# Optimization experiments

Measured on AMD Instinct MI355X. Metric: run time of the kernel, lower is better.

## Reference

```python
import jax, jax.numpy as jnp
import numpy as np

B, S, D, H = 2, 2048, 1024, 16
HD = D // H               # head_dim = input_size / num_heads
STEPS = 1                 # update_steps_max extra Hopfield update steps
LN_EPS = 1e-5
SCALING = 1.0 / np.sqrt(HD)  # beta = 1/sqrt(head_dim)


def layernorm(x, g, b):
    m = x.mean(-1, keepdims=True)
    v = ((x - m) ** 2).mean(-1, keepdims=True)
    return (x - m) * jax.lax.rsqrt(v + LN_EPS) * g + b


def setup_inputs() -> dict:
    key = jax.random.key(0)
    ks = jax.random.split(key, 9)
    s = 0.02
    f32 = jnp.float32
    return {
        "data": jax.random.normal(ks[0], (B, S, D), f32),
        # affine LayerNorm params (stored / state / projection patterns)
        "g_k": jnp.ones((D,), f32), "b_k": jnp.zeros((D,), f32),
        "g_q": jnp.ones((D,), f32), "b_q": jnp.zeros((D,), f32),
        "g_v": jnp.ones((D,), f32), "b_v": jnp.zeros((D,), f32),
        # in-projections (q/k/v) and out-projection of HopfieldCore
        "Wq": jax.random.normal(ks[1], (D, D), f32) * s, "bq": jnp.zeros((D,), f32),
        "Wk": jax.random.normal(ks[2], (D, D), f32) * s, "bk": jnp.zeros((D,), f32),
        "Wv": jax.random.normal(ks[3], (D, D), f32) * s, "bv": jnp.zeros((D,), f32),
        "Wo": jax.random.normal(ks[4], (D, D), f32) * s, "bo": jnp.zeros((D,), f32),
    }


def reference(data, g_k, b_k, g_q, b_q, g_v, b_v,
              Wq, bq, Wk, bk, Wv, bv, Wo, bo):
    # single input tensor used as stored / state / projection pattern
    xk = layernorm(data, g_k, b_k)   # stored pattern  -> keys
    xq = layernorm(data, g_q, b_q)   # state pattern   -> queries
    xv = layernorm(data, g_v, b_v)   # pattern proj    -> values

    split = lambda t: t.reshape(B, S, H, HD).transpose(0, 2, 1, 3)  # [B,H,S,HD]
    q = split(xq @ Wq + bq)
    k = split(xk @ Wk + bk)
    v = split(xv @ Wv + bv)

    def assoc(q):  # xi = softmax(beta * q K^T)
        return jax.nn.softmax(
            jnp.einsum('bhqd,bhkd->bhqk', q, k) * SCALING, axis=-1)

    xi = assoc(q)
    for _ in range(STEPS):           # iterative Hopfield update: q <- xi K
        q = jnp.einsum('bhqk,bhkd->bhqd', xi, k)
        xi = assoc(q)

    out = jnp.einsum('bhqk,bhkd->bhqd', xi, v)        # retrieve with values
    out = out.transpose(0, 2, 1, 3).reshape(B, S, D)  # merge heads
    return out @ Wo + bo
```

## Files before the change

### kernel.cpp

```cpp
#include <hip/hip_runtime.h>
#include <hip/hip_bf16.h>

#define B_  2
#define S_  2048
#define D_  1024
#define H_  16
#define HD_ 64
#define M_  4096


typedef __attribute__((ext_vector_type(8))) short short8;
typedef __attribute__((ext_vector_type(4))) float f32x4;

#define CE_ 0.1803368801111204f
#define SD_ 56

typedef __attribute__((address_space(1))) const unsigned GU;
typedef __attribute__((address_space(3))) unsigned LU;
static __device__ __forceinline__ void glds16(const void* g, void* l){
  __builtin_amdgcn_global_load_lds((GU*)g, (LU*)l, 16, 0, 0);
}

static __device__ __forceinline__ unsigned short f2bfc(float f){
  union{float f; unsigned u;} c; c.f = f;
  return (unsigned short)((c.u + 0x8000u) >> 16);
}
static __device__ __forceinline__ unsigned pk2bf(float a, float b){
  union{float f; unsigned u;} ca, cb; ca.f=a; cb.f=b;
  return __builtin_amdgcn_perm(cb.u + 0x8000u, ca.u + 0x8000u, 0x07060302u);
}
static __device__ __forceinline__ unsigned pk2bft(float a, float b){
  union{float f; unsigned u;} ca, cb; ca.f=a; cb.f=b;
  return __builtin_amdgcn_perm(cb.u, ca.u, 0x07060302u);
}

__global__ __launch_bounds__(256) void prep_kernel(
  const float* __restrict__ data,
  const float* __restrict__ Wq, const float* __restrict__ Wk,
  const float* __restrict__ Wv, const float* __restrict__ Wo,
  const float* __restrict__ gq, const float* __restrict__ gk, const float* __restrict__ gv,
  const float* __restrict__ blq, const float* __restrict__ blk, const float* __restrict__ blv,
  const float* __restrict__ bpq, const float* __restrict__ bpk, const float* __restrict__ bpv,
  unsigned short* __restrict__ WT, unsigned short* __restrict__ xhat,
  float* __restrict__ bf)
{
  __shared__ unsigned short tile[64][72];
  __shared__ float red[4][64];
  int bid = blockIdx.x, t = threadIdx.x;
  if (bid < 1024){
    int z = bid >> 8, rem = bid & 255;
    int k0 = (rem>>4)*64, n0 = (rem&15)*64;
    const float* W = (z==0)?Wq:(z==1)?Wk:(z==2)?Wv:Wo;
    const float* g = (z==0)?gq:(z==1)?gk:(z==2)?gv:(const float*)0;
    unsigned short* out = WT + ((size_t)z<<20);
    {
      int kr = t>>2, c16 = (t&3)*16;
      float gs = g ? g[k0+kr]*((z==0)?CE_:1.0f) : 1.0f;
      const float* src = W + (size_t)(k0+kr)*D_ + n0 + c16;
      float4 w0 = *(const float4*)(src);
      float4 w1 = *(const float4*)(src+4);
      float4 w2 = *(const float4*)(src+8);
      float4 w3 = *(const float4*)(src+12);
      unsigned* tp = (unsigned*)&tile[kr][c16];
      tp[0]=pk2bf(w0.x*gs,w0.y*gs); tp[1]=pk2bf(w0.z*gs,w0.w*gs);
      tp[2]=pk2bf(w1.x*gs,w1.y*gs); tp[3]=pk2bf(w1.z*gs,w1.w*gs);
      tp[4]=pk2bf(w2.x*gs,w2.y*gs); tp[5]=pk2bf(w2.z*gs,w2.w*gs);
      tp[6]=pk2bf(w3.x*gs,w3.y*gs); tp[7]=pk2bf(w3.z*gs,w3.w*gs);
    }
    __syncthreads();
    {
      int nr = t>>2, kc = (t&3)*16;
      union { uint4 v[2]; unsigned short u[16]; } st;
      #pragma unroll
      for (int i=0;i<16;i++) st.u[i] = tile[kc+i][nr];
      unsigned short* dst = out + (size_t)(n0+nr)*D_ + k0 + kc;
      *(uint4*)(dst)     = st.v[0];
      *(uint4*)(dst + 8) = st.v[1];
    }
  } else if (bid < 2048){
    int row = (bid-1024)*4 + (t>>6);
    int l = t & 63;
    const float4* xr = (const float4*)(data + (size_t)row*D_);
    float4 v[4];
    float s = 0.f, ss = 0.f;
    #pragma unroll
    for (int i=0;i<4;i++){
      v[i] = xr[l + 64*i];
      s  += v[i].x+v[i].y+v[i].z+v[i].w;
      ss += v[i].x*v[i].x+v[i].y*v[i].y+v[i].z*v[i].z+v[i].w*v[i].w;
    }
    #pragma unroll
    for (int m=1;m<64;m<<=1){ s += __shfl_xor(s, m, 64); ss += __shfl_xor(ss, m, 64); }
    float me = s*(1.0f/D_);
    float var = ss*(1.0f/D_) - me*me;
    float rs = rsqrtf(var + 1e-5f);
    float nm = -me*rs;
    unsigned short* xo = xhat + (size_t)row*D_;
    #pragma unroll
    for (int i=0;i<4;i++){
      uint2 pk;
      pk.x = pk2bf(fmaf(v[i].x,rs,nm), fmaf(v[i].y,rs,nm));
      pk.y = pk2bf(fmaf(v[i].z,rs,nm), fmaf(v[i].w,rs,nm));
      *(uint2*)(xo + 4*l + 256*i) = pk;
    }
  } else {
    int idx = bid - 2048;
    int z = idx >> 4, xb = idx & 15;
    const float* W  = (z==0)?Wq:(z==1)?Wk:Wv;
    const float* bl = (z==0)?blq:(z==1)?blk:blv;
    const float* bp = (z==0)?bpq:(z==1)?bpk:bpv;
    int nl = t & 63, kg = t >> 6;
    int n = xb*64 + nl;
    float acc = 0.f;
    for (int k = kg*256; k < (kg+1)*256; k++)
      acc += bl[k] * W[(size_t)k*D_ + n];
    red[kg][nl] = acc;
    __syncthreads();
    if (t < 64){
      int nn = xb*64 + t;
      float v = red[0][t]+red[1][t]+red[2][t]+red[3][t] + bp[nn];
      bf[z*D_ + nn] = (z==0) ? v*CE_ : v;
    }
  }
}

__global__ __launch_bounds__(256) void gemm_qkv(
  const unsigned short* __restrict__ xhat,
  const unsigned short* __restrict__ WT,
  const float* __restrict__ biasf,
  unsigned short* __restrict__ qv, unsigned short* __restrict__ kb,
  unsigned short* __restrict__ kT, unsigned short* __restrict__ vT)
{
  int z = blockIdx.z;
  const unsigned short* Bt = WT + ((size_t)z<<20);
  const float* bias = biasf + z*D_;
  unsigned short* oN = (z==0)?qv:(z==1)?kb:(unsigned short*)0;
  unsigned short* oT = (z==0)?(unsigned short*)0:(z==1)?kT:vT;

  __shared__ __align__(16) unsigned short As[128*32];
  __shared__ __align__(16) unsigned short Bs[128*32];
  int tid = threadIdx.x, w = tid>>6, l = tid&63;
  int m0 = blockIdx.x*128, n0 = blockIdx.y*128;
  int wr = (w>>1)*64, wc = (w&1)*64;
  int lr = l&15, qd = l>>4;

  const unsigned short* gA = xhat + (size_t)(m0 + w*32 + (l>>2))*D_ + (l&3)*8;
  const unsigned short* gB = Bt   + (size_t)(n0 + w*32 + (l>>2))*D_ + (l&3)*8;
  unsigned short* lA0 = &As[(w*32)*32];
  unsigned short* lA1 = &As[(w*32+16)*32];
  unsigned short* lB0 = &Bs[(w*32)*32];
  unsigned short* lB1 = &Bs[(w*32+16)*32];

  const f32x4 fz = {0.f,0.f,0.f,0.f};
  f32x4 acc[4][4];
  #pragma unroll
  for (int i=0;i<4;i++)
    #pragma unroll
    for (int j=0;j<4;j++) acc[i][j] = fz;

  for (int kk=0; kk<D_; kk+=32){
    __syncthreads();
    glds16(gA + kk,                 lA0);
    glds16(gA + kk + (size_t)16*D_, lA1);
    glds16(gB + kk,                 lB0);
    glds16(gB + kk + (size_t)16*D_, lB1);
    __syncthreads();
    short8 af[4], bfr[4];
    #pragma unroll
    for (int i=0;i<4;i++) af[i]  = *(const short8*)(As + (wr + i*16 + lr)*32 + qd*8);
    #pragma unroll
    for (int j=0;j<4;j++) bfr[j] = *(const short8*)(Bs + (wc + j*16 + lr)*32 + qd*8);
    #pragma unroll
    for (int i=0;i<4;i++)
      #pragma unroll
      for (int j=0;j<4;j++)
        acc[i][j] = __builtin_amdgcn_mfma_f32_16x16x32_bf16(af[i], bfr[j], acc[i][j], 0, 0, 0);
  }

  #pragma unroll
  for (int j=0;j<4;j++){
    int n = n0 + wc + j*16 + lr;
    float bias_n = bias[n];
    #pragma unroll
    for (int i=0;i<4;i++){
      int mb = m0 + wr + i*16 + qd*4;
      float v0 = acc[i][j][0] + bias_n;
      float v1 = acc[i][j][1] + bias_n;
      float v2 = acc[i][j][2] + bias_n;
      float v3 = acc[i][j][3] + bias_n;
      if (oN){
        oN[(size_t)(mb+0)*D_ + n] = f2bfc(v0);
        oN[(size_t)(mb+1)*D_ + n] = f2bfc(v1);
        oN[(size_t)(mb+2)*D_ + n] = f2bfc(v2);
        oN[(size_t)(mb+3)*D_ + n] = f2bfc(v3);
      }
      if (oT){
        int bb = mb >> 11, sI = mb & (S_-1);
        int hh = n >> 6,  dd = n & 63;
        uint2 pk; pk.x = pk2bf(v0, v1); pk.y = pk2bf(v2, v3);
        *(uint2*)(oT + (size_t)((bb*H_ + hh)*HD_ + dd)*S_ + sI) = pk;
      }
    }
  }
}

__global__ __launch_bounds__(256) void gemm_out(
  const unsigned short* __restrict__ A,
  const unsigned short* __restrict__ Bt,
  const float* __restrict__ bo,
  float* __restrict__ Cf)
{
  __shared__ __align__(16) unsigned short As[128*32];
  __shared__ __align__(16) unsigned short Bs[128*32];
  int tid = threadIdx.x, w = tid>>6, l = tid&63;
  int m0 = blockIdx.x*128, n0 = blockIdx.y*128;
  int wr = (w>>1)*64, wc = (w&1)*64;
  int lr = l&15, qd = l>>4;

  const unsigned short* gA = A  + (size_t)(m0 + w*32 + (l>>2))*D_ + (l&3)*8;
  const unsigned short* gB = Bt + (size_t)(n0 + w*32 + (l>>2))*D_ + (l&3)*8;
  unsigned short* lA0 = &As[(w*32)*32];
  unsigned short* lA1 = &As[(w*32+16)*32];
  unsigned short* lB0 = &Bs[(w*32)*32];
  unsigned short* lB1 = &Bs[(w*32+16)*32];

  const f32x4 fz = {0.f,0.f,0.f,0.f};
  f32x4 acc[4][4];
  #pragma unroll
  for (int i=0;i<4;i++)
    #pragma unroll
    for (int j=0;j<4;j++) acc[i][j] = fz;

  for (int kk=0; kk<D_; kk+=32){
    __syncthreads();
    glds16(gA + kk,                 lA0);
    glds16(gA + kk + (size_t)16*D_, lA1);
    glds16(gB + kk,                 lB0);
    glds16(gB + kk + (size_t)16*D_, lB1);
    __syncthreads();
    short8 af[4], bfr[4];
    #pragma unroll
    for (int i=0;i<4;i++) af[i]  = *(const short8*)(As + (wr + i*16 + lr)*32 + qd*8);
    #pragma unroll
    for (int j=0;j<4;j++) bfr[j] = *(const short8*)(Bs + (wc + j*16 + lr)*32 + qd*8);
    #pragma unroll
    for (int i=0;i<4;i++)
      #pragma unroll
      for (int j=0;j<4;j++)
        acc[i][j] = __builtin_amdgcn_mfma_f32_16x16x32_bf16(af[i], bfr[j], acc[i][j], 0, 0, 0);
  }

  #pragma unroll
  for (int j=0;j<4;j++){
    int n = n0 + wc + j*16 + lr;
    float bias_n = bo[n];
    #pragma unroll
    for (int i=0;i<4;i++){
      int mb = m0 + wr + i*16 + qd*4;
      Cf[(size_t)(mb+0)*D_ + n] = acc[i][j][0] + bias_n;
      Cf[(size_t)(mb+1)*D_ + n] = acc[i][j][1] + bias_n;
      Cf[(size_t)(mb+2)*D_ + n] = acc[i][j][2] + bias_n;
      Cf[(size_t)(mb+3)*D_ + n] = acc[i][j][3] + bias_n;
    }
  }
}

__global__ __launch_bounds__(256) void attn_fused(
  unsigned short* __restrict__ QO,
  const unsigned short* __restrict__ K,
  const unsigned short* __restrict__ KT,
  const unsigned short* __restrict__ VT)
{
  int qt = blockIdx.x;
  int h  = blockIdx.y;
  int b  = qt >> 4;
  int bh = b*H_ + h;
  int tid = threadIdx.x, w = tid>>6, l = tid&63;
  int lr = l&15, qd = l>>4;
  int r8 = tid>>3, c8 = (tid&7)*8;
  int chf = c8>>5, co = c8&31;

  __shared__ __align__(16) unsigned short sK[2][64*SD_];
  __shared__ __align__(16) unsigned short sV[2][64*SD_];
  __shared__ __align__(16) unsigned short sP[4][2][16*SD_];

  const f32x4 fz = {0.f,0.f,0.f,0.f};

  unsigned short* Qbase = QO + (size_t)(qt*128 + w*32) * D_ + h*64;
  short8 qf[2][2];
  #pragma unroll
  for (int gg=0; gg<2; gg++)
    #pragma unroll
    for (int hf=0; hf<2; hf++)
      qf[gg][hf] = *(const short8*)(Qbase + (size_t)(gg*16+lr)*D_ + hf*32 + qd*8);

  const unsigned short* Khead = K + (size_t)(b*S_)*D_ + h*64;
  const unsigned short* Vh0 = KT + (size_t)bh*HD_*S_;
  const unsigned short* Vh1 = VT + (size_t)bh*HD_*S_;
  unsigned short* Pw0 = &sP[w][0][0];
  unsigned short* Pw1 = &sP[w][1][0];

  f32x4 oacc[2][4];
  float lac[2];

  uint4 kr0, kr1, vr0, vr1;
  {
    kr0 = *(const uint4*)(Khead + (size_t)(r8   )*D_ + c8);
    kr1 = *(const uint4*)(Khead + (size_t)(r8+32)*D_ + c8);
    vr0 = *(const uint4*)(Vh0 + (size_t)(r8   )*S_ + c8);
    vr1 = *(const uint4*)(Vh0 + (size_t)(r8+32)*S_ + c8);
  }

  #pragma unroll 1
  for (int phase=0; phase<2; phase++){
    const unsigned short* Vhead = phase ? Vh1 : Vh0;
    lac[0]=0.f; lac[1]=0.f;
    #pragma unroll
    for (int gg=0;gg<2;gg++)
      #pragma unroll
      for (int t=0;t<4;t++) oacc[gg][t]=fz;

    for (int kt=0; kt<S_; kt+=64){
      __syncthreads();
      *(uint4*)(&sK[chf][(r8   )*SD_ + co]) = kr0;
      *(uint4*)(&sK[chf][(r8+32)*SD_ + co]) = kr1;
      *(uint4*)(&sV[chf][(r8   )*SD_ + co]) = vr0;
      *(uint4*)(&sV[chf][(r8+32)*SD_ + co]) = vr1;
      __syncthreads();

      {
        int nkt = kt + 64;
        const unsigned short* Vn = Vhead;
        if (nkt >= S_){ nkt = 0; Vn = Vh1; }
        kr0 = *(const uint4*)(Khead + (size_t)(nkt+r8   )*D_ + c8);
        kr1 = *(const uint4*)(Khead + (size_t)(nkt+r8+32)*D_ + c8);
        vr0 = *(const uint4*)(Vn + (size_t)(r8   )*S_ + nkt + c8);
        vr1 = *(const uint4*)(Vn + (size_t)(r8+32)*S_ + nkt + c8);
      }

      f32x4 sc[2][4];
      #pragma unroll
      for (int st=0; st<4; st++){
        short8 kA0 = *(const short8*)(&sK[0][(st*16+lr)*SD_ + qd*8]);
        short8 kA1 = *(const short8*)(&sK[1][(st*16+lr)*SD_ + qd*8]);
        #pragma unroll
        for (int gg=0; gg<2; gg++){
          f32x4 z = fz;
          z = __builtin_amdgcn_mfma_f32_16x16x32_bf16(kA0, qf[gg][0], z, 0,0,0);
          z = __builtin_amdgcn_mfma_f32_16x16x32_bf16(kA1, qf[gg][1], z, 0,0,0);
          sc[gg][st] = z;
        }
      }
      short8 pf[2][2];
      #pragma unroll
      for (int gg=0; gg<2; gg++){
        #pragma unroll
        for (int st=0; st<4; st++){
          float p0=__builtin_amdgcn_exp2f(sc[gg][st][0]);
          float p1=__builtin_amdgcn_exp2f(sc[gg][st][1]);
          float p2=__builtin_amdgcn_exp2f(sc[gg][st][2]);
          float p3=__builtin_amdgcn_exp2f(sc[gg][st][3]);
          lac[gg] += (p0+p1)+(p2+p3);
          uint2 pk; pk.x = pk2bft(p0,p1); pk.y = pk2bft(p2,p3);
          unsigned short* Ph = (st&2) ? Pw1 : Pw0;
          *(uint2*)(Ph + lr*SD_ + (st&1)*16 + qd*4) = pk;
        }
        pf[gg][0] = *(const short8*)(Pw0 + lr*SD_ + qd*8);
        pf[gg][1] = *(const short8*)(Pw1 + lr*SD_ + qd*8);
      }
      #pragma unroll
      for (int dt=0; dt<4; dt++){
        short8 vA0 = *(const short8*)(&sV[0][(dt*16+lr)*SD_ + qd*8]);
        short8 vA1 = *(const short8*)(&sV[1][(dt*16+lr)*SD_ + qd*8]);
        #pragma unroll
        for (int gg=0; gg<2; gg++){
          oacc[gg][dt] = __builtin_amdgcn_mfma_f32_16x16x32_bf16(vA0, pf[gg][0], oacc[gg][dt], 0,0,0);
          oacc[gg][dt] = __builtin_amdgcn_mfma_f32_16x16x32_bf16(vA1, pf[gg][1], oacc[gg][dt], 0,0,0);
        }
      }
    }

    #pragma unroll
    for (int gg=0;gg<2;gg++){
      lac[gg] += __shfl_xor(lac[gg], 16, 64);
      lac[gg] += __shfl_xor(lac[gg], 32, 64);
    }

    if (phase==0){
      #pragma unroll
      for (int gg=0;gg<2;gg++){
        float iv = CE_ * __builtin_amdgcn_rcpf(lac[gg]);
        #pragma unroll
        for (int dt=0;dt<4;dt++){
          uint2 pk;
          pk.x = pk2bf(oacc[gg][dt][0]*iv, oacc[gg][dt][1]*iv);
          pk.y = pk2bf(oacc[gg][dt][2]*iv, oacc[gg][dt][3]*iv);
          unsigned short* Ph = (dt&2) ? Pw1 : Pw0;
          *(uint2*)(Ph + lr*SD_ + (dt&1)*16 + qd*4) = pk;
        }
        qf[gg][0] = *(const short8*)(Pw0 + lr*SD_ + qd*8);
        qf[gg][1] = *(const short8*)(Pw1 + lr*SD_ + qd*8);
      }
    } else {
      #pragma unroll
      for (int gg=0;gg<2;gg++){
        float iv = __builtin_amdgcn_rcpf(lac[gg]);
        unsigned short* Ob = QO + (size_t)(qt*128 + w*32 + gg*16 + lr)*D_ + h*64;
        #pragma unroll
        for (int dt=0;dt<4;dt++){
          uint2 pk;
          pk.x = pk2bf(oacc[gg][dt][0]*iv, oacc[gg][dt][1]*iv);
          pk.y = pk2bf(oacc[gg][dt][2]*iv, oacc[gg][dt][3]*iv);
          *(uint2*)(Ob + dt*16 + qd*4) = pk;
        }
      }
    }
  }
}

extern "C" void kernel_launch(void* const* d_in, const int* in_sizes, int n_in,
                              void* d_out, int out_size, void* d_ws, size_t ws_size,
                              hipStream_t stream){
  const float* data = (const float*)d_in[0];
  const float* g_k  = (const float*)d_in[1];
  const float* b_k  = (const float*)d_in[2];
  const float* g_q  = (const float*)d_in[3];
  const float* b_q  = (const float*)d_in[4];
  const float* g_v  = (const float*)d_in[5];
  const float* b_v  = (const float*)d_in[6];
  const float* Wq   = (const float*)d_in[7];
  const float* bq   = (const float*)d_in[8];
  const float* Wk   = (const float*)d_in[9];
  const float* bk   = (const float*)d_in[10];
  const float* Wv   = (const float*)d_in[11];
  const float* bv   = (const float*)d_in[12];
  const float* Wo   = (const float*)d_in[13];
  const float* bo   = (const float*)d_in[14];
  float* out = (float*)d_out;

  char* ws = (char*)d_ws;
  const size_t MB = (size_t)1<<20;
  unsigned short* q    = (unsigned short*)(ws);
  unsigned short* kb   = (unsigned short*)(ws + 8*MB);
  unsigned short* WT   = (unsigned short*)(ws + 16*MB);
  unsigned short* WTo  = WT + ((size_t)3<<20);
  unsigned short* xhat = (unsigned short*)(ws + 24*MB);
  float*          bfld = (float*)(ws + 32*MB);
  unsigned short* vT   = (unsigned short*)d_out;
  unsigned short* kT   = (unsigned short*)((char*)d_out + 8*MB);

  dim3 gb(256);
  prep_kernel<<<dim3(2096), gb, 0, stream>>>(data,
                                             Wq, Wk, Wv, Wo, g_q, g_k, g_v,
                                             b_q, b_k, b_v, bq, bk, bv,
                                             WT, xhat, bfld);
  gemm_qkv<<<dim3(32,8,3), gb, 0, stream>>>(xhat, WT, bfld, q, kb, kT, vT);
  attn_fused<<<dim3(32, H_), gb, 0, stream>>>(q, kb, kT, vT);
  gemm_out<<<dim3(32,8), gb, 0, stream>>>(q, WTo, bo, out);
}
```

Measured before the change: 271.0 us.

## Switch attention to 32x32x16 MFMA with register P transpose via permlane32 swap

The fused attention kernel moves from 16x16x32 to 32x32x16 bf16 MFMA tiles with S^T layout, so each wave holds 32 queries in one accumulator set. The probability and normalised-query operands are repacked in registers with permlane32_swap instead of a round trip through shared memory. The K/V shared tiles drop their padding in favour of an XOR swizzle. The row sum is computed with an extra MFMA against a ones vector. This cuts LDS traffic and VALU reductions, at the cost of an extra MFMA per k-step and higher register pressure from 16-wide accumulators.

```diff
diff --git a/kernel.cpp b/kernel.cpp
--- a/kernel.cpp
+++ b/kernel.cpp
@@ -11,9 +11,9 @@
 
 typedef __attribute__((ext_vector_type(8))) short short8;
 typedef __attribute__((ext_vector_type(4))) float f32x4;
+typedef __attribute__((ext_vector_type(16))) float f32x16;
 
 #define CE_ 0.1803368801111204f
-#define SD_ 56
 
 typedef __attribute__((address_space(1))) const unsigned GU;
 typedef __attribute__((address_space(3))) unsigned LU;
@@ -32,6 +32,15 @@
 static __device__ __forceinline__ unsigned pk2bft(float a, float b){
   union{float f; unsigned u;} ca, cb; ca.f=a; cb.f=b;
   return __builtin_amdgcn_perm(cb.u, ca.u, 0x07060302u);
+}
+static __device__ __forceinline__ short8 mk8(unsigned x0, unsigned x1,
+                                             unsigned x2, unsigned x3){
+  union{ unsigned u[4]; short8 s; } t;
+  t.u[0]=x0; t.u[1]=x1; t.u[2]=x2; t.u[3]=x3; return t.s;
+}
+static __device__ __forceinline__ void plswap(unsigned &x, unsigned &y){
+  auto r = __builtin_amdgcn_permlane32_swap(x, y, false, false);
+  x = (unsigned)r[0]; y = (unsigned)r[1];
 }
 
 __global__ __launch_bounds__(256) void prep_kernel(
@@ -276,56 +285,47 @@
   int b  = qt >> 4;
   int bh = b*H_ + h;
   int tid = threadIdx.x, w = tid>>6, l = tid&63;
-  int lr = l&15, qd = l>>4;
+  int lq = l & 31;
+  int hi = l >> 5;
   int r8 = tid>>3, c8 = (tid&7)*8;
-  int chf = c8>>5, co = c8&31;
-
-  __shared__ __align__(16) unsigned short sK[2][64*SD_];
-  __shared__ __align__(16) unsigned short sV[2][64*SD_];
-  __shared__ __align__(16) unsigned short sP[4][2][16*SD_];
-
-  const f32x4 fz = {0.f,0.f,0.f,0.f};
-
-  unsigned short* Qbase = QO + (size_t)(qt*128 + w*32) * D_ + h*64;
-  short8 qf[2][2];
+  int swzw = (r8&7)<<3;
+  int swzr = (lq&7)<<3;
+
+  __shared__ __align__(16) unsigned short sK[64*64];
+  __shared__ __align__(16) unsigned short sV[64*64];
+
+  const f32x16 fz16 = {0.f,0.f,0.f,0.f,0.f,0.f,0.f,0.f,
+                       0.f,0.f,0.f,0.f,0.f,0.f,0.f,0.f};
+  const short8 ones = {(short)0x3F80,(short)0x3F80,(short)0x3F80,(short)0x3F80,
+                       (short)0x3F80,(short)0x3F80,(short)0x3F80,(short)0x3F80};
+
+  const unsigned short* Qb = QO + (size_t)(qt*128 + w*32 + lq)*D_ + h*64;
+  short8 qf[4];
   #pragma unroll
-  for (int gg=0; gg<2; gg++)
-    #pragma unroll
-    for (int hf=0; hf<2; hf++)
-      qf[gg][hf] = *(const short8*)(Qbase + (size_t)(gg*16+lr)*D_ + hf*32 + qd*8);
+  for (int d=0; d<4; d++)
+    qf[d] = *(const short8*)(Qb + d*16 + hi*8);
 
   const unsigned short* Khead = K + (size_t)(b*S_)*D_ + h*64;
   const unsigned short* Vh0 = KT + (size_t)bh*HD_*S_;
   const unsigned short* Vh1 = VT + (size_t)bh*HD_*S_;
-  unsigned short* Pw0 = &sP[w][0][0];
-  unsigned short* Pw1 = &sP[w][1][0];
-
-  f32x4 oacc[2][4];
-  float lac[2];
 
   uint4 kr0, kr1, vr0, vr1;
-  {
-    kr0 = *(const uint4*)(Khead + (size_t)(r8   )*D_ + c8);
-    kr1 = *(const uint4*)(Khead + (size_t)(r8+32)*D_ + c8);
-    vr0 = *(const uint4*)(Vh0 + (size_t)(r8   )*S_ + c8);
-    vr1 = *(const uint4*)(Vh0 + (size_t)(r8+32)*S_ + c8);
-  }
+  kr0 = *(const uint4*)(Khead + (size_t)(r8   )*D_ + c8);
+  kr1 = *(const uint4*)(Khead + (size_t)(r8+32)*D_ + c8);
+  vr0 = *(const uint4*)(Vh0 + (size_t)(r8   )*S_ + c8);
+  vr1 = *(const uint4*)(Vh0 + (size_t)(r8+32)*S_ + c8);
 
   #pragma unroll 1
   for (int phase=0; phase<2; phase++){
     const unsigned short* Vhead = phase ? Vh1 : Vh0;
-    lac[0]=0.f; lac[1]=0.f;
-    #pragma unroll
-    for (int gg=0;gg<2;gg++)
-      #pragma unroll
-      for (int t=0;t<4;t++) oacc[gg][t]=fz;
+    f32x16 oacc0 = fz16, oacc1 = fz16, lacc = fz16;
 
     for (int kt=0; kt<S_; kt+=64){
       __syncthreads();
-      *(uint4*)(&sK[chf][(r8   )*SD_ + co]) = kr0;
-      *(uint4*)(&sK[chf][(r8+32)*SD_ + co]) = kr1;
-      *(uint4*)(&sV[chf][(r8   )*SD_ + co]) = vr0;
-      *(uint4*)(&sV[chf][(r8+32)*SD_ + co]) = vr1;
+      *(uint4*)(&sK[(size_t)(r8   )*64 + (c8 ^ swzw)]) = kr0;
+      *(uint4*)(&sK[(size_t)(r8+32)*64 + (c8 ^ swzw)]) = kr1;
+      *(uint4*)(&sV[(size_t)(r8   )*64 + (c8 ^ swzw)]) = vr0;
+      *(uint4*)(&sV[(size_t)(r8+32)*64 + (c8 ^ swzw)]) = vr1;
       __syncthreads();
 
       {
@@ -338,81 +338,83 @@
         vr1 = *(const uint4*)(Vn + (size_t)(r8+32)*S_ + nkt + c8);
       }
 
-      f32x4 sc[2][4];
-      #pragma unroll
-      for (int st=0; st<4; st++){
-        short8 kA0 = *(const short8*)(&sK[0][(st*16+lr)*SD_ + qd*8]);
-        short8 kA1 = *(const short8*)(&sK[1][(st*16+lr)*SD_ + qd*8]);
-        #pragma unroll
-        for (int gg=0; gg<2; gg++){
-          f32x4 z = fz;
-          z = __builtin_amdgcn_mfma_f32_16x16x32_bf16(kA0, qf[gg][0], z, 0,0,0);
-          z = __builtin_amdgcn_mfma_f32_16x16x32_bf16(kA1, qf[gg][1], z, 0,0,0);
-          sc[gg][st] = z;
-        }
-      }
-      short8 pf[2][2];
-      #pragma unroll
-      for (int gg=0; gg<2; gg++){
-        #pragma unroll
-        for (int st=0; st<4; st++){
-          float p0=__builtin_amdgcn_exp2f(sc[gg][st][0]);
-          float p1=__builtin_amdgcn_exp2f(sc[gg][st][1]);
-          float p2=__builtin_amdgcn_exp2f(sc[gg][st][2]);
-          float p3=__builtin_amdgcn_exp2f(sc[gg][st][3]);
-          lac[gg] += (p0+p1)+(p2+p3);
-          uint2 pk; pk.x = pk2bft(p0,p1); pk.y = pk2bft(p2,p3);
-          unsigned short* Ph = (st&2) ? Pw1 : Pw0;
-          *(uint2*)(Ph + lr*SD_ + (st&1)*16 + qd*4) = pk;
-        }
-        pf[gg][0] = *(const short8*)(Pw0 + lr*SD_ + qd*8);
-        pf[gg][1] = *(const short8*)(Pw1 + lr*SD_ + qd*8);
-      }
-      #pragma unroll
-      for (int dt=0; dt<4; dt++){
-        short8 vA0 = *(const short8*)(&sV[0][(dt*16+lr)*SD_ + qd*8]);
-        short8 vA1 = *(const short8*)(&sV[1][(dt*16+lr)*SD_ + qd*8]);
-        #pragma unroll
-        for (int gg=0; gg<2; gg++){
-          oacc[gg][dt] = __builtin_amdgcn_mfma_f32_16x16x32_bf16(vA0, pf[gg][0], oacc[gg][dt], 0,0,0);
-          oacc[gg][dt] = __builtin_amdgcn_mfma_f32_16x16x32_bf16(vA1, pf[gg][1], oacc[gg][dt], 0,0,0);
-        }
-      }
-    }
-
-    #pragma unroll
-    for (int gg=0;gg<2;gg++){
-      lac[gg] += __shfl_xor(lac[gg], 16, 64);
-      lac[gg] += __shfl_xor(lac[gg], 32, 64);
+      f32x16 sc0 = fz16, sc1 = fz16;
+      #pragma unroll
+      for (int ds_=0; ds_<4; ds_++){
+        short8 ka0 = *(const short8*)(&sK[(size_t)(lq   )*64 + ((ds_*16 + hi*8) ^ swzr)]);
+        short8 ka1 = *(const short8*)(&sK[(size_t)(lq+32)*64 + ((ds_*16 + hi*8) ^ swzr)]);
+        sc0 = __builtin_amdgcn_mfma_f32_32x32x16_bf16(ka0, qf[ds_], sc0, 0,0,0);
+        sc1 = __builtin_amdgcn_mfma_f32_32x32x16_bf16(ka1, qf[ds_], sc1, 0,0,0);
+      }
+
+      float p0[16], p1[16];
+      #pragma unroll
+      for (int i=0;i<16;i++){
+        p0[i] = __builtin_amdgcn_exp2f(sc0[i]);
+        p1[i] = __builtin_amdgcn_exp2f(sc1[i]);
+      }
+      short8 pf[4];
+      {
+        unsigned a0,a1,b0,b1;
+        a0=pk2bft(p0[0],p0[1]);   a1=pk2bft(p0[2],p0[3]);
+        b0=pk2bft(p0[4],p0[5]);   b1=pk2bft(p0[6],p0[7]);
+        plswap(a0,b0); plswap(a1,b1);
+        pf[0] = mk8(a0,a1,b0,b1);
+        a0=pk2bft(p0[8],p0[9]);   a1=pk2bft(p0[10],p0[11]);
+        b0=pk2bft(p0[12],p0[13]); b1=pk2bft(p0[14],p0[15]);
+        plswap(a0,b0); plswap(a1,b1);
+        pf[1] = mk8(a0,a1,b0,b1);
+        a0=pk2bft(p1[0],p1[1]);   a1=pk2bft(p1[2],p1[3]);
+        b0=pk2bft(p1[4],p1[5]);   b1=pk2bft(p1[6],p1[7]);
+        plswap(a0,b0); plswap(a1,b1);
+        pf[2] = mk8(a0,a1,b0,b1);
+        a0=pk2bft(p1[8],p1[9]);   a1=pk2bft(p1[10],p1[11]);
+        b0=pk2bft(p1[12],p1[13]); b1=pk2bft(p1[14],p1[15]);
+        plswap(a0,b0); plswap(a1,b1);
+        pf[3] = mk8(a0,a1,b0,b1);
+      }
+
+      #pragma unroll
+      for (int ks=0; ks<4; ks++){
+        short8 va0 = *(const short8*)(&sV[(size_t)(lq   )*64 + ((ks*16 + hi*8) ^ swzr)]);
+        short8 va1 = *(const short8*)(&sV[(size_t)(lq+32)*64 + ((ks*16 + hi*8) ^ swzr)]);
+        oacc0 = __builtin_amdgcn_mfma_f32_32x32x16_bf16(va0, pf[ks], oacc0, 0,0,0);
+        oacc1 = __builtin_amdgcn_mfma_f32_32x32x16_bf16(va1, pf[ks], oacc1, 0,0,0);
+        lacc  = __builtin_amdgcn_mfma_f32_32x32x16_bf16(ones, pf[ks], lacc, 0,0,0);
+      }
     }
 
     if (phase==0){
-      #pragma unroll
-      for (int gg=0;gg<2;gg++){
-        float iv = CE_ * __builtin_amdgcn_rcpf(lac[gg]);
-        #pragma unroll
-        for (int dt=0;dt<4;dt++){
-          uint2 pk;
-          pk.x = pk2bf(oacc[gg][dt][0]*iv, oacc[gg][dt][1]*iv);
-          pk.y = pk2bf(oacc[gg][dt][2]*iv, oacc[gg][dt][3]*iv);
-          unsigned short* Ph = (dt&2) ? Pw1 : Pw0;
-          *(uint2*)(Ph + lr*SD_ + (dt&1)*16 + qd*4) = pk;
-        }
-        qf[gg][0] = *(const short8*)(Pw0 + lr*SD_ + qd*8);
-        qf[gg][1] = *(const short8*)(Pw1 + lr*SD_ + qd*8);
-      }
+      float iv = CE_ * __builtin_amdgcn_rcpf(lacc[0]);
+      unsigned a0,a1,b0,b1;
+      a0=pk2bf(oacc0[0]*iv, oacc0[1]*iv);   a1=pk2bf(oacc0[2]*iv, oacc0[3]*iv);
+      b0=pk2bf(oacc0[4]*iv, oacc0[5]*iv);   b1=pk2bf(oacc0[6]*iv, oacc0[7]*iv);
+      plswap(a0,b0); plswap(a1,b1);
+      qf[0] = mk8(a0,a1,b0,b1);
+      a0=pk2bf(oacc0[8]*iv, oacc0[9]*iv);   a1=pk2bf(oacc0[10]*iv, oacc0[11]*iv);
+      b0=pk2bf(oacc0[12]*iv, oacc0[13]*iv); b1=pk2bf(oacc0[14]*iv, oacc0[15]*iv);
+      plswap(a0,b0); plswap(a1,b1);
+      qf[1] = mk8(a0,a1,b0,b1);
+      a0=pk2bf(oacc1[0]*iv, oacc1[1]*iv);   a1=pk2bf(oacc1[2]*iv, oacc1[3]*iv);
+      b0=pk2bf(oacc1[4]*iv, oacc1[5]*iv);   b1=pk2bf(oacc1[6]*iv, oacc1[7]*iv);
+      plswap(a0,b0); plswap(a1,b1);
+      qf[2] = mk8(a0,a1,b0,b1);
+      a0=pk2bf(oacc1[8]*iv, oacc1[9]*iv);   a1=pk2bf(oacc1[10]*iv, oacc1[11]*iv);
+      b0=pk2bf(oacc1[12]*iv, oacc1[13]*iv); b1=pk2bf(oacc1[14]*iv, oacc1[15]*iv);
+      plswap(a0,b0); plswap(a1,b1);
+      qf[3] = mk8(a0,a1,b0,b1);
     } else {
-      #pragma unroll
-      for (int gg=0;gg<2;gg++){
-        float iv = __builtin_amdgcn_rcpf(lac[gg]);
-        unsigned short* Ob = QO + (size_t)(qt*128 + w*32 + gg*16 + lr)*D_ + h*64;
-        #pragma unroll
-        for (int dt=0;dt<4;dt++){
-          uint2 pk;
-          pk.x = pk2bf(oacc[gg][dt][0]*iv, oacc[gg][dt][1]*iv);
-          pk.y = pk2bf(oacc[gg][dt][2]*iv, oacc[gg][dt][3]*iv);
-          *(uint2*)(Ob + dt*16 + qd*4) = pk;
-        }
+      float iv = __builtin_amdgcn_rcpf(lacc[0]);
+      unsigned short* Ob = QO + (size_t)(qt*128 + w*32 + lq)*D_ + h*64 + hi*4;
+      #pragma unroll
+      for (int g=0; g<4; g++){
+        uint2 pk;
+        pk.x = pk2bf(oacc0[4*g+0]*iv, oacc0[4*g+1]*iv);
+        pk.y = pk2bf(oacc0[4*g+2]*iv, oacc0[4*g+3]*iv);
+        *(uint2*)(Ob + g*8) = pk;
+        pk.x = pk2bf(oacc1[4*g+0]*iv, oacc1[4*g+1]*iv);
+        pk.y = pk2bf(oacc1[4*g+2]*iv, oacc1[4*g+3]*iv);
+        *(uint2*)(Ob + 32 + g*8) = pk;
       }
     }
   }
```

After: 256.5 us. 5.4% less time.
